# Performance work log

Hardware: AMD Instinct MI355X
Metric: run time of the kernel (lower is better)

The kernel has to match this reference:

```python
import jax, jax.numpy as jnp
import numpy as np

NUM_HEADS = 16
D_K = 64
D_V = 64
D_MODEL = 1024


def setup_inputs() -> dict:
    key = jax.random.key(0)
    ks = jax.random.split(key, 11)
    B, S = 2, 2048
    s = 0.02
    return {
        "Q": jax.random.normal(ks[0], (B, S, D_MODEL), jnp.float32),
        "K": jax.random.normal(ks[1], (B, S, D_MODEL), jnp.float32),
        "V": jax.random.normal(ks[2], (B, S, D_MODEL), jnp.float32),
        "WQ": jax.random.normal(ks[3], (D_MODEL, NUM_HEADS * D_K), jnp.float32) * s,
        "bQ": jnp.zeros((NUM_HEADS * D_K,), jnp.float32),
        "WK": jax.random.normal(ks[4], (D_MODEL, NUM_HEADS * D_K), jnp.float32) * s,
        "bK": jnp.zeros((NUM_HEADS * D_K,), jnp.float32),
        "WV": jax.random.normal(ks[5], (D_MODEL, NUM_HEADS * D_V), jnp.float32) * s,
        "bV": jnp.zeros((NUM_HEADS * D_V,), jnp.float32),
        "WO": jax.random.normal(ks[6], (NUM_HEADS * D_V, D_MODEL), jnp.float32) * s,
        "bO": jnp.zeros((D_MODEL,), jnp.float32),
    }


def reference(Q, K, V, WQ, bQ, WK, bK, WV, bV, WO, bO):
    B = Q.shape[0]
    # linear projections, then split heads: [B, H, S, d]
    q = (Q @ WQ + bQ).reshape(B, -1, NUM_HEADS, D_K).transpose(0, 2, 1, 3)
    k = (K @ WK + bK).reshape(B, -1, NUM_HEADS, D_K).transpose(0, 2, 1, 3)
    v = (V @ WV + bV).reshape(B, -1, NUM_HEADS, D_V).transpose(0, 2, 1, 3)
    # unfused attention: full [B, H, Sq, Sk] score matrix
    scores = jnp.einsum("bhqd,bhkd->bhqk", q, k) / jnp.sqrt(jnp.float32(D_K))
    attn = jax.nn.softmax(scores, axis=-1)  # dropout is identity in eval mode
    out = jnp.einsum("bhqk,bhkd->bhqd", attn, v)
    out = out.transpose(0, 2, 1, 3).reshape(B, -1, NUM_HEADS * D_V)
    return out @ WO + bO
```

## Files before the change

### kernel.cpp

```cpp
#include <hip/hip_runtime.h>
#include <hip/hip_bf16.h>
#include <stdint.h>

#define BATCH 2
#define SEQ   2048
#define NH    16
#define DH    64
#define DM    1024
#define MR    (BATCH * SEQ)

typedef __bf16 bf16_t;
typedef bf16_t bf16x4 __attribute__((ext_vector_type(4)));
typedef bf16_t bf16x8 __attribute__((ext_vector_type(8)));
typedef float  f32x4  __attribute__((ext_vector_type(4)));
typedef float  f32x16 __attribute__((ext_vector_type(16)));

typedef const __attribute__((address_space(1))) void* gas_t;
typedef       __attribute__((address_space(3))) void* las_t;

__device__ __forceinline__ void gload16(const void* g, void* l) {
  __builtin_amdgcn_global_load_lds((gas_t)g, (las_t)l, 16, 0, 0);
}

__device__ __forceinline__ float fast_exp2(float x) {
#if __has_builtin(__builtin_amdgcn_exp2f)
  return __builtin_amdgcn_exp2f(x);
#else
  float r; asm volatile("v_exp_f32 %0, %1\n\ts_nop 1" : "=v"(r) : "v"(x)); return r;
#endif
}

__global__ __launch_bounds__(256) void cvt3_kernel(const float* __restrict__ x0,
                                                   const float* __restrict__ x1,
                                                   const float* __restrict__ x2,
                                                   bf16_t* __restrict__ y0,
                                                   bf16_t* __restrict__ y1,
                                                   bf16_t* __restrict__ y2, int n) {
  const int z = blockIdx.y;
  const float* x = z == 0 ? x0 : (z == 1 ? x1 : x2);
  bf16_t*      y = z == 0 ? y0 : (z == 1 ? y1 : y2);
  int i = (blockIdx.x * 256 + threadIdx.x) * 8;
  if (i + 8 <= n) {
    float4 a = *(const float4*)(x + i);
    float4 b = *(const float4*)(x + i + 4);
    bf16x8 o;
    o[0] = (bf16_t)a.x; o[1] = (bf16_t)a.y; o[2] = (bf16_t)a.z; o[3] = (bf16_t)a.w;
    o[4] = (bf16_t)b.x; o[5] = (bf16_t)b.y; o[6] = (bf16_t)b.z; o[7] = (bf16_t)b.w;
    *(bf16x8*)(y + i) = o;
  }
}

__global__ __launch_bounds__(256) void wtrans4_kernel(const float* __restrict__ W0,
                                                      const float* __restrict__ W1,
                                                      const float* __restrict__ W2,
                                                      const float* __restrict__ W3,
                                                      bf16_t* __restrict__ T0,
                                                      bf16_t* __restrict__ T1,
                                                      bf16_t* __restrict__ T2,
                                                      bf16_t* __restrict__ T3) {
  const int z = blockIdx.z;
  const float* W = z == 0 ? W0 : (z == 1 ? W1 : (z == 2 ? W2 : W3));
  bf16_t*     Wt = z == 0 ? T0 : (z == 1 ? T1 : (z == 2 ? T2 : T3));
  __shared__ bf16_t t[64][65];
  const int c0 = blockIdx.x * 64, r0 = blockIdx.y * 64;
  const int tid = threadIdx.x;
  const int r = tid >> 2, cc = (tid & 3) * 16;
  const float* src = W + (size_t)(r0 + r) * DM + c0 + cc;
#pragma unroll
  for (int i = 0; i < 16; ++i) t[r][cc + i] = (bf16_t)src[i];
  __syncthreads();
  bf16_t* dst = Wt + (size_t)(c0 + r) * DM + r0 + cc;
#pragma unroll
  for (int i = 0; i < 16; ++i) dst[i] = t[cc + i][r];
}

__global__ __launch_bounds__(256) void vtrans_kernel(const bf16_t* __restrict__ v,
                                                     bf16_t* __restrict__ vT) {
  __shared__ bf16_t t[64][65];
  const int s0 = blockIdx.x * 64;
  const int h = blockIdx.y, b = blockIdx.z;
  const int tid = threadIdx.x;
  const int r = tid >> 2, cc = (tid & 3) * 16;
  const bf16_t* src = v + (size_t)(b * SEQ + s0 + r) * DM + h * DH + cc;
#pragma unroll
  for (int i = 0; i < 16; ++i) t[r][cc + i] = src[i];
  __syncthreads();
  bf16_t* dst = vT + (size_t)((b * NH + h) * DH + r) * SEQ + s0 + cc;
#pragma unroll
  for (int i = 0; i < 16; ++i) dst[i] = t[cc + i][r];
}

__global__ __launch_bounds__(256) void gemm3_kernel(
    const bf16_t* __restrict__ A0, const bf16_t* __restrict__ A1,
    const bf16_t* __restrict__ A2,
    const bf16_t* __restrict__ B0, const bf16_t* __restrict__ B1,
    const bf16_t* __restrict__ B2,
    const float* __restrict__ bi0, const float* __restrict__ bi1,
    const float* __restrict__ bi2,
    float s0, float s1, float s2,
    bf16_t* __restrict__ C0, bf16_t* __restrict__ C1, bf16_t* __restrict__ C2) {
  const int z = blockIdx.z;
  const bf16_t* A    = z == 0 ? A0 : (z == 1 ? A1 : A2);
  const bf16_t* Bt   = z == 0 ? B0 : (z == 1 ? B1 : B2);
  const float*  bias = z == 0 ? bi0 : (z == 1 ? bi1 : bi2);
  const float   scale = z == 0 ? s0 : (z == 1 ? s1 : s2);
  bf16_t*       C    = z == 0 ? C0 : (z == 1 ? C1 : C2);
  const int K = DM, N = DM;

  __shared__ __attribute__((aligned(16))) bf16_t As[128 * 64];
  __shared__ __attribute__((aligned(16))) bf16_t Bs[128 * 64];
  const int m0 = blockIdx.x * 128, n0 = blockIdx.y * 128;
  const int tid = threadIdx.x;
  const int wave = tid >> 6, lane = tid & 63;
  const int lm = lane & 15, lg = lane >> 4;
  const int wr = wave >> 1, wc = wave & 1;
  f32x4 acc[4][4];
#pragma unroll
  for (int a = 0; a < 4; ++a)
#pragma unroll
    for (int bb = 0; bb < 4; ++bb) acc[a][bb] = (f32x4){0.f, 0.f, 0.f, 0.f};

  for (int k0 = 0; k0 < K; k0 += 64) {
    __syncthreads();
#pragma unroll
    for (int i = 0; i < 4; ++i) {
      const int c = tid + i * 256;
      const int row = c >> 3, j = c & 7, js = j ^ (row & 7);
      gload16(A  + (size_t)(m0 + row) * K + k0 + js * 8,
              As + (size_t)(wave * 64 + i * 256) * 8);
      gload16(Bt + (size_t)(n0 + row) * K + k0 + js * 8,
              Bs + (size_t)(wave * 64 + i * 256) * 8);
    }
    asm volatile("s_waitcnt vmcnt(0)" ::: "memory");
    __syncthreads();
#pragma unroll
    for (int kk = 0; kk < 2; ++kk) {
      bf16x8 af[4], bfr[4];
#pragma unroll
      for (int t = 0; t < 4; ++t) {
        const int ra = wr * 64 + t * 16 + lm;
        af[t] = *(const bf16x8*)((const char*)As + ra * 128 +
                                 ((kk * 64 + lg * 16) ^ ((ra & 7) << 4)));
        const int rb = wc * 64 + t * 16 + lm;
        bfr[t] = *(const bf16x8*)((const char*)Bs + rb * 128 +
                                  ((kk * 64 + lg * 16) ^ ((rb & 7) << 4)));
      }
      __builtin_amdgcn_s_setprio(1);
#pragma unroll
      for (int mf = 0; mf < 4; ++mf)
#pragma unroll
        for (int nf = 0; nf < 4; ++nf)
          acc[mf][nf] = __builtin_amdgcn_mfma_f32_16x16x32_bf16(af[mf], bfr[nf],
                                                                acc[mf][nf], 0, 0, 0);
      __builtin_amdgcn_s_setprio(0);
    }
  }
#pragma unroll
  for (int mf = 0; mf < 4; ++mf)
#pragma unroll
    for (int nf = 0; nf < 4; ++nf) {
      const int col = n0 + wc * 64 + nf * 16 + lm;
      const float bv = bias[col];
#pragma unroll
      for (int i = 0; i < 4; ++i) {
        const int row = m0 + wr * 64 + mf * 16 + lg * 4 + i;
        C[(size_t)row * N + col] = (bf16_t)((acc[mf][nf][i] + bv) * scale);
      }
    }
}

template <int OUT_BF16>
__global__ __launch_bounds__(256) void gemm_kernel(const bf16_t* __restrict__ A,
                                                   const bf16_t* __restrict__ Bt,
                                                   const float* __restrict__ bias,
                                                   float scale,
                                                   void* __restrict__ Cv,
                                                   int K, int N) {
  __shared__ __attribute__((aligned(16))) bf16_t As[64 * 64];
  __shared__ __attribute__((aligned(16))) bf16_t Bs[128 * 64];
  const int m0 = blockIdx.x * 64, n0 = blockIdx.y * 128;
  const int tid = threadIdx.x;
  const int wave = tid >> 6, lane = tid & 63;
  const int lm = lane & 15, lg = lane >> 4;
  const int wr = wave >> 1, wc = wave & 1;
  f32x4 acc[2][4];
#pragma unroll
  for (int a = 0; a < 2; ++a)
#pragma unroll
    for (int bb = 0; bb < 4; ++bb) acc[a][bb] = (f32x4){0.f, 0.f, 0.f, 0.f};

  for (int k0 = 0; k0 < K; k0 += 64) {
    __syncthreads();
#pragma unroll
    for (int i = 0; i < 2; ++i) {
      const int c = tid + i * 256;
      const int row = c >> 3, j = c & 7, js = j ^ (row & 7);
      gload16(A + (size_t)(m0 + row) * K + k0 + js * 8,
              As + (size_t)(wave * 64 + i * 256) * 8);
    }
#pragma unroll
    for (int i = 0; i < 4; ++i) {
      const int c = tid + i * 256;
      const int row = c >> 3, j = c & 7, js = j ^ (row & 7);
      gload16(Bt + (size_t)(n0 + row) * K + k0 + js * 8,
              Bs + (size_t)(wave * 64 + i * 256) * 8);
    }
    asm volatile("s_waitcnt vmcnt(0)" ::: "memory");
    __syncthreads();
#pragma unroll
    for (int kk = 0; kk < 2; ++kk) {
      bf16x8 af[2], bfr[4];
#pragma unroll
      for (int t = 0; t < 2; ++t) {
        const int ra = wr * 32 + t * 16 + lm;
        af[t] = *(const bf16x8*)((const char*)As + ra * 128 +
                                 ((kk * 64 + lg * 16) ^ ((ra & 7) << 4)));
      }
#pragma unroll
      for (int t = 0; t < 4; ++t) {
        const int rb = wc * 64 + t * 16 + lm;
        bfr[t] = *(const bf16x8*)((const char*)Bs + rb * 128 +
                                  ((kk * 64 + lg * 16) ^ ((rb & 7) << 4)));
      }
      __builtin_amdgcn_s_setprio(1);
#pragma unroll
      for (int mf = 0; mf < 2; ++mf)
#pragma unroll
        for (int nf = 0; nf < 4; ++nf)
          acc[mf][nf] = __builtin_amdgcn_mfma_f32_16x16x32_bf16(af[mf], bfr[nf],
                                                                acc[mf][nf], 0, 0, 0);
      __builtin_amdgcn_s_setprio(0);
    }
  }
#pragma unroll
  for (int mf = 0; mf < 2; ++mf)
#pragma unroll
    for (int nf = 0; nf < 4; ++nf) {
      const int col = n0 + wc * 64 + nf * 16 + lm;
      const float bv = bias[col];
#pragma unroll
      for (int i = 0; i < 4; ++i) {
        const int row = m0 + wr * 32 + mf * 16 + lg * 4 + i;
        const float val = (acc[mf][nf][i] + bv) * scale;
        if (OUT_BF16) ((bf16_t*)Cv)[(size_t)row * N + col] = (bf16_t)val;
        else          ((float*)Cv)[(size_t)row * N + col] = val;
      }
    }
}

__global__ __launch_bounds__(256, 3) void flash_kernel(const bf16_t* __restrict__ q,
                                                       const bf16_t* __restrict__ k,
                                                       const bf16_t* __restrict__ vT,
                                                       bf16_t* __restrict__ o) {
  __shared__ __attribute__((aligned(16))) bf16_t Ks[2][64 * 64];
  __shared__ __attribute__((aligned(16))) bf16_t Vs[2][64 * 64];
  __shared__ __attribute__((aligned(16))) bf16_t Ps[4][32 * 64];
  const int wg = blockIdx.x;
  const int swz = (wg & 7) * 64 + (wg >> 3);
  const int qt = swz & 15, h = (swz >> 4) & 15, b = swz >> 8;
  const int tid = threadIdx.x;
  const int wave = tid >> 6, lane = tid & 63;
  const int lq = lane & 31, hi = lane >> 5;
  char* PsW = (char*)(&Ps[wave][0]);

  const bf16_t* qb = q + (size_t)(b * SEQ + qt * 128 + wave * 32) * DM + h * DH;
  const int c0r = tid >> 3,  c0j = (tid & 7) ^ (c0r & 7);
  const int c1r = c0r + 32,  c1j = (tid & 7) ^ (c1r & 7);
  const bf16_t* kbase = k + (size_t)b * SEQ * DM + h * DH;
  const bf16_t* vbase = vT + (size_t)(b * NH + h) * DH * SEQ;
  const bf16_t* ks0 = kbase + (size_t)c0r * DM + c0j * 8;
  const bf16_t* ks1 = kbase + (size_t)c1r * DM + c1j * 8;
  const bf16_t* vs0 = vbase + (size_t)c0r * SEQ + c0j * 8;
  const bf16_t* vs1 = vbase + (size_t)c1r * SEQ + c1j * 8;

  bf16x8 qf[4];
#pragma unroll
  for (int ds = 0; ds < 4; ++ds)
    qf[ds] = *(const bf16x8*)(qb + (size_t)lq * DM + ds * 16 + hi * 8);

  f32x16 acc[2];
#pragma unroll
  for (int r = 0; r < 16; ++r) { acc[0][r] = 0.f; acc[1][r] = 0.f; }
  float mrun = -1e30f, lrun = 0.f;

  gload16(ks0, &Ks[0][(wave * 64) * 8]);
  gload16(ks1, &Ks[0][(wave * 64 + 256) * 8]);
  gload16(vs0, &Vs[0][(wave * 64) * 8]);
  gload16(vs1, &Vs[0][(wave * 64 + 256) * 8]);

  const int NT = SEQ / 64;
  for (int t = 0; t < NT; ++t) {
    const int cur = t & 1;
    asm volatile("" ::: "memory");
    __builtin_amdgcn_s_barrier();
    if (t + 1 < NT) {
      const int nb = cur ^ 1;
      gload16(ks0 + (size_t)(t + 1) * 64 * DM, &Ks[nb][(wave * 64) * 8]);
      gload16(ks1 + (size_t)(t + 1) * 64 * DM, &Ks[nb][(wave * 64 + 256) * 8]);
      gload16(vs0 + (t + 1) * 64,              &Vs[nb][(wave * 64) * 8]);
      gload16(vs1 + (t + 1) * 64,              &Vs[nb][(wave * 64 + 256) * 8]);
      asm volatile("s_waitcnt vmcnt(4)" ::: "memory");
    } else {
      asm volatile("s_waitcnt vmcnt(0)" ::: "memory");
    }
    __builtin_amdgcn_s_barrier();
    asm volatile("" ::: "memory");

    const char* Kb_ = (const char*)&Ks[cur][0];
    const char* Vb_ = (const char*)&Vs[cur][0];

    f32x16 sc[2];
#pragma unroll
    for (int r = 0; r < 16; ++r) { sc[0][r] = 0.f; sc[1][r] = 0.f; }
    __builtin_amdgcn_s_setprio(1);
#pragma unroll
    for (int ds = 0; ds < 4; ++ds) {
#pragma unroll
      for (int kt = 0; kt < 2; ++kt) {
        const int row = kt * 32 + lq;
        bf16x8 kfrag = *(const bf16x8*)(Kb_ + row * 128 +
                                        ((ds * 32 + hi * 16) ^ ((row & 7) << 4)));
        sc[kt] = __builtin_amdgcn_mfma_f32_32x32x16_bf16(kfrag, qf[ds], sc[kt], 0, 0, 0);
      }
    }
    __builtin_amdgcn_s_setprio(0);

    float ml = sc[0][0];
#pragma unroll
    for (int r = 1; r < 16; ++r) ml = fmaxf(ml, sc[0][r]);
#pragma unroll
    for (int r = 0; r < 16; ++r) ml = fmaxf(ml, sc[1][r]);
    ml = fmaxf(ml, __shfl_xor(ml, 32));
    const bool defer = __all(ml - mrun <= 8.0f);
    const float mn = defer ? mrun : fmaxf(mrun, ml);
#pragma unroll
    for (int kt = 0; kt < 2; ++kt)
#pragma unroll
      for (int r = 0; r < 16; ++r) sc[kt][r] = fast_exp2(sc[kt][r] - mn);
    float s = 0.f;
#pragma unroll
    for (int r = 0; r < 16; ++r) s += sc[0][r] + sc[1][r];
    s += __shfl_xor(s, 32);
    if (defer) {
      lrun += s;
    } else {
      const float alpha = fast_exp2(mrun - mn);
      mrun = mn;
      lrun = lrun * alpha + s;
#pragma unroll
      for (int r = 0; r < 16; ++r) {
        const float ar = __shfl(alpha, (r & 3) + 8 * (r >> 2) + 4 * hi);
        acc[0][r] *= ar;
        acc[1][r] *= ar;
      }
    }

#pragma unroll
    for (int kt = 0; kt < 2; ++kt)
#pragma unroll
      for (int g = 0; g < 4; ++g) {
        bf16x4 pw;
        pw[0] = (bf16_t)sc[kt][4 * g + 0]; pw[1] = (bf16_t)sc[kt][4 * g + 1];
        pw[2] = (bf16_t)sc[kt][4 * g + 2]; pw[3] = (bf16_t)sc[kt][4 * g + 3];
        *(bf16x4*)(PsW + lq * 128 +
                   ((kt * 64 + g * 16 + hi * 8) ^ ((lq & 7) << 4))) = pw;
      }

#pragma unroll
    for (int ks = 0; ks < 4; ++ks) {
      bf16x8 pf = *(const bf16x8*)(PsW + lq * 128 +
                                   ((ks * 32 + hi * 16) ^ ((lq & 7) << 4)));
      __builtin_amdgcn_s_setprio(1);
#pragma unroll
      for (int dt = 0; dt < 2; ++dt) {
        const int row = dt * 32 + lq;
        bf16x8 vfrag = *(const bf16x8*)(Vb_ + row * 128 +
                                        ((ks * 32 + hi * 16) ^ ((row & 7) << 4)));
        acc[dt] = __builtin_amdgcn_mfma_f32_32x32x16_bf16(pf, vfrag, acc[dt], 0, 0, 0);
      }
      __builtin_amdgcn_s_setprio(0);
    }
  }

  const float inv = __builtin_amdgcn_rcpf(lrun);
#pragma unroll
  for (int r = 0; r < 16; ++r) {
    const int qrow = (r & 3) + 8 * (r >> 2) + 4 * hi;
    const float iv = __shfl(inv, qrow);
    const int row = b * SEQ + qt * 128 + wave * 32 + qrow;
#pragma unroll
    for (int dt = 0; dt < 2; ++dt) {
      const int col = h * DH + dt * 32 + lq;
      o[(size_t)row * DM + col] = (bf16_t)(acc[dt][r] * iv);
    }
  }
}

extern "C" void kernel_launch(void* const* d_in, const int* in_sizes, int n_in,
                              void* d_out, int out_size, void* d_ws, size_t ws_size,
                              hipStream_t stream) {
  (void)in_sizes; (void)n_in; (void)out_size; (void)ws_size;
  const float* Q  = (const float*)d_in[0];
  const float* Kx = (const float*)d_in[1];
  const float* V  = (const float*)d_in[2];
  const float* WQ = (const float*)d_in[3];
  const float* bQ = (const float*)d_in[4];
  const float* WK = (const float*)d_in[5];
  const float* bK = (const float*)d_in[6];
  const float* WV = (const float*)d_in[7];
  const float* bV = (const float*)d_in[8];
  const float* WO = (const float*)d_in[9];
  const float* bO = (const float*)d_in[10];

  const size_t MS  = (size_t)MR * DM;
  const size_t WSZ = (size_t)DM * DM;
  bf16_t* ws  = (bf16_t*)d_ws;
  bf16_t* Qb  = ws;
  bf16_t* Kb  = Qb + MS;
  bf16_t* Vb  = Kb + MS;
  bf16_t* WQt = Vb + MS;
  bf16_t* WKt = WQt + WSZ;
  bf16_t* WVt = WKt + WSZ;
  bf16_t* WOt = WVt + WSZ;
  bf16_t* qp  = WOt + WSZ;
  bf16_t* kp  = qp + MS;
  bf16_t* vp  = kp + MS;
  bf16_t* vTb = Qb;
  bf16_t* ao  = Kb;

  const float scale_q = 0.125f * 1.44269504088896340736f;

  cvt3_kernel<<<dim3((unsigned)(MS / 2048), 3), 256, 0, stream>>>(Q, Kx, V, Qb, Kb, Vb, (int)MS);
  wtrans4_kernel<<<dim3(16, 16, 4), 256, 0, stream>>>(WQ, WK, WV, WO, WQt, WKt, WVt, WOt);

  gemm3_kernel<<<dim3(32, 8, 3), 256, 0, stream>>>(Qb, Kb, Vb,
                                                   WQt, WKt, WVt,
                                                   bQ, bK, bV,
                                                   scale_q, 1.0f, 1.0f,
                                                   qp, kp, vp);

  vtrans_kernel<<<dim3(SEQ / 64, NH, BATCH), 256, 0, stream>>>(vp, vTb);
  flash_kernel<<<dim3(512), 256, 0, stream>>>(qp, kp, vTb, ao);
  gemm_kernel<0><<<dim3(MR / 64, DM / 128), 256, 0, stream>>>(ao, WOt, bO, 1.0f, d_out, DM, DM);
}
```

Baseline: 138.6 us.

## Write K/V in MFMA-fragment layout from projection GEMM; load directly to registers in flash

The QKV projection epilogue now writes K and V in a per-head layout that already matches the MFMA fragment order, which makes the separate V-transpose kernel unnecessary. The flash kernel drops its shared-memory K/V double buffering and barriers. Each wave instead loads K and V fragments straight from global memory into registers, with K software-prefetched one tile ahead. The cost is that every wave of a block reloads the same K/V from global or L2 instead of sharing it through LDS, register pressure rises (launch bounds go from 3 to 2 blocks), and the epilogue stores become scattered.

```diff
diff --git a/kernel.cpp b/kernel.cpp
--- a/kernel.cpp
+++ b/kernel.cpp
@@ -74,22 +74,6 @@
   for (int i = 0; i < 16; ++i) dst[i] = t[cc + i][r];
 }
 
-__global__ __launch_bounds__(256) void vtrans_kernel(const bf16_t* __restrict__ v,
-                                                     bf16_t* __restrict__ vT) {
-  __shared__ bf16_t t[64][65];
-  const int s0 = blockIdx.x * 64;
-  const int h = blockIdx.y, b = blockIdx.z;
-  const int tid = threadIdx.x;
-  const int r = tid >> 2, cc = (tid & 3) * 16;
-  const bf16_t* src = v + (size_t)(b * SEQ + s0 + r) * DM + h * DH + cc;
-#pragma unroll
-  for (int i = 0; i < 16; ++i) t[r][cc + i] = src[i];
-  __syncthreads();
-  bf16_t* dst = vT + (size_t)((b * NH + h) * DH + r) * SEQ + s0 + cc;
-#pragma unroll
-  for (int i = 0; i < 16; ++i) dst[i] = t[cc + i][r];
-}
-
 __global__ __launch_bounds__(256) void gemm3_kernel(
     const bf16_t* __restrict__ A0, const bf16_t* __restrict__ A1,
     const bf16_t* __restrict__ A2,
@@ -164,7 +148,23 @@
 #pragma unroll
       for (int i = 0; i < 4; ++i) {
         const int row = m0 + wr * 64 + mf * 16 + lg * 4 + i;
-        C[(size_t)row * N + col] = (bf16_t)((acc[mf][nf][i] + bv) * scale);
+        const float val = (acc[mf][nf][i] + bv) * scale;
+        size_t off;
+        if (z == 0) {
+          off = (size_t)row * N + col;
+        } else {
+          const int bb = row >> 11, s = row & (SEQ - 1);
+          const int hh = col >> 6, d = col & 63;
+          const size_t base = (size_t)(bb * NH + hh) * (SEQ * DH);
+          if (z == 1) {
+            off = base + ((((size_t)(s >> 6) * 2 + ((s >> 5) & 1)) * 4 + (d >> 4)) * 64
+                          + ((d >> 3) & 1) * 32 + (s & 31)) * 8 + (d & 7);
+          } else {
+            off = base + ((((size_t)(s >> 6) * 2 + (d >> 5)) * 4 + ((s >> 4) & 3)) * 64
+                          + ((s >> 3) & 1) * 32 + (d & 31)) * 8 + (s & 7);
+          }
+        }
+        C[off] = (bf16_t)val;
       }
     }
 }
@@ -248,12 +248,84 @@
     }
 }
 
-__global__ __launch_bounds__(256, 3) void flash_kernel(const bf16_t* __restrict__ q,
-                                                       const bf16_t* __restrict__ k,
-                                                       const bf16_t* __restrict__ vT,
+__device__ __forceinline__ void attn_iter5(const bf16x8 (&kf)[8],
+                                           const bf16x8 (&qf)[4],
+                                           const bf16_t* __restrict__ vbt,
+                                           f32x16 (&acc0)[2],
+                                           float& mrun, float& lrun,
+                                           char* __restrict__ PsW,
+                                           int lq, int hi, int lane) {
+  bf16x8 vf[8];
+#pragma unroll
+  for (int i = 0; i < 8; ++i) vf[i] = *(const bf16x8*)(vbt + i * 512);
+
+  f32x16 sc[2];
+#pragma unroll
+  for (int r = 0; r < 16; ++r) { sc[0][r] = 0.f; sc[1][r] = 0.f; }
+  __builtin_amdgcn_s_setprio(1);
+#pragma unroll
+  for (int ds = 0; ds < 4; ++ds) {
+    sc[0] = __builtin_amdgcn_mfma_f32_32x32x16_bf16(kf[ds],     qf[ds], sc[0], 0, 0, 0);
+    sc[1] = __builtin_amdgcn_mfma_f32_32x32x16_bf16(kf[4 + ds], qf[ds], sc[1], 0, 0, 0);
+  }
+  __builtin_amdgcn_s_setprio(0);
+
+  float ml = sc[0][0];
+#pragma unroll
+  for (int r = 1; r < 16; ++r) ml = fmaxf(ml, sc[0][r]);
+#pragma unroll
+  for (int r = 0; r < 16; ++r) ml = fmaxf(ml, sc[1][r]);
+  ml = fmaxf(ml, __shfl_xor(ml, 32));
+  const bool defer = __all(ml - mrun <= 8.0f);
+  const float mn = defer ? mrun : fmaxf(mrun, ml);
+#pragma unroll
+  for (int kt = 0; kt < 2; ++kt)
+#pragma unroll
+    for (int r = 0; r < 16; ++r) sc[kt][r] = fast_exp2(sc[kt][r] - mn);
+  float s = 0.f;
+#pragma unroll
+  for (int r = 0; r < 16; ++r) s += sc[0][r] + sc[1][r];
+  s += __shfl_xor(s, 32);
+  if (defer) {
+    lrun += s;
+  } else {
+    const float alpha = fast_exp2(mrun - mn);
+    mrun = mn;
+    lrun = lrun * alpha + s;
+#pragma unroll
+    for (int r = 0; r < 16; ++r) {
+      const float ar = __shfl(alpha, (r & 3) + 8 * (r >> 2) + 4 * hi);
+      acc0[0][r] *= ar;
+      acc0[1][r] *= ar;
+    }
+  }
+
+#pragma unroll
+  for (int kt = 0; kt < 2; ++kt)
+#pragma unroll
+    for (int g = 0; g < 4; ++g) {
+      bf16x4 pw;
+      pw[0] = (bf16_t)sc[kt][4 * g + 0]; pw[1] = (bf16_t)sc[kt][4 * g + 1];
+      pw[2] = (bf16_t)sc[kt][4 * g + 2]; pw[3] = (bf16_t)sc[kt][4 * g + 3];
+      *(bf16x4*)(PsW + lq * 128 +
+                 ((kt * 64 + g * 16 + hi * 8) ^ ((lq & 7) << 4))) = pw;
+    }
+
+#pragma unroll
+  for (int ks = 0; ks < 4; ++ks) {
+    bf16x8 pf = *(const bf16x8*)(PsW + lq * 128 +
+                                 ((ks * 32 + hi * 16) ^ ((lq & 7) << 4)));
+    __builtin_amdgcn_s_setprio(1);
+    acc0[0] = __builtin_amdgcn_mfma_f32_32x32x16_bf16(pf, vf[ks],     acc0[0], 0, 0, 0);
+    acc0[1] = __builtin_amdgcn_mfma_f32_32x32x16_bf16(pf, vf[4 + ks], acc0[1], 0, 0, 0);
+    __builtin_amdgcn_s_setprio(0);
+  }
+}
+
+__global__ __launch_bounds__(256, 2) void flash_kernel(const bf16_t* __restrict__ q,
+                                                       const bf16_t* __restrict__ kF,
+                                                       const bf16_t* __restrict__ vF,
                                                        bf16_t* __restrict__ o) {
-  __shared__ __attribute__((aligned(16))) bf16_t Ks[2][64 * 64];
-  __shared__ __attribute__((aligned(16))) bf16_t Vs[2][64 * 64];
   __shared__ __attribute__((aligned(16))) bf16_t Ps[4][32 * 64];
   const int wg = blockIdx.x;
   const int swz = (wg & 7) * 64 + (wg >> 3);
@@ -264,14 +336,8 @@
   char* PsW = (char*)(&Ps[wave][0]);
 
   const bf16_t* qb = q + (size_t)(b * SEQ + qt * 128 + wave * 32) * DM + h * DH;
-  const int c0r = tid >> 3,  c0j = (tid & 7) ^ (c0r & 7);
-  const int c1r = c0r + 32,  c1j = (tid & 7) ^ (c1r & 7);
-  const bf16_t* kbase = k + (size_t)b * SEQ * DM + h * DH;
-  const bf16_t* vbase = vT + (size_t)(b * NH + h) * DH * SEQ;
-  const bf16_t* ks0 = kbase + (size_t)c0r * DM + c0j * 8;
-  const bf16_t* ks1 = kbase + (size_t)c1r * DM + c1j * 8;
-  const bf16_t* vs0 = vbase + (size_t)c0r * SEQ + c0j * 8;
-  const bf16_t* vs1 = vbase + (size_t)c1r * SEQ + c1j * 8;
+  const bf16_t* kb = kF + (size_t)(b * NH + h) * (SEQ * DH) + lane * 8;
+  const bf16_t* vb = vF + (size_t)(b * NH + h) * (SEQ * DH) + lane * 8;
 
   bf16x8 qf[4];
 #pragma unroll
@@ -283,103 +349,23 @@
   for (int r = 0; r < 16; ++r) { acc[0][r] = 0.f; acc[1][r] = 0.f; }
   float mrun = -1e30f, lrun = 0.f;
 
-  gload16(ks0, &Ks[0][(wave * 64) * 8]);
-  gload16(ks1, &Ks[0][(wave * 64 + 256) * 8]);
-  gload16(vs0, &Vs[0][(wave * 64) * 8]);
-  gload16(vs1, &Vs[0][(wave * 64 + 256) * 8]);
+  bf16x8 kfA[8], kfB[8];
+#pragma unroll
+  for (int i = 0; i < 8; ++i) kfA[i] = *(const bf16x8*)(kb + i * 512);
 
   const int NT = SEQ / 64;
-  for (int t = 0; t < NT; ++t) {
-    const int cur = t & 1;
-    asm volatile("" ::: "memory");
-    __builtin_amdgcn_s_barrier();
-    if (t + 1 < NT) {
-      const int nb = cur ^ 1;
-      gload16(ks0 + (size_t)(t + 1) * 64 * DM, &Ks[nb][(wave * 64) * 8]);
-      gload16(ks1 + (size_t)(t + 1) * 64 * DM, &Ks[nb][(wave * 64 + 256) * 8]);
-      gload16(vs0 + (t + 1) * 64,              &Vs[nb][(wave * 64) * 8]);
-      gload16(vs1 + (t + 1) * 64,              &Vs[nb][(wave * 64 + 256) * 8]);
-      asm volatile("s_waitcnt vmcnt(4)" ::: "memory");
-    } else {
-      asm volatile("s_waitcnt vmcnt(0)" ::: "memory");
-    }
-    __builtin_amdgcn_s_barrier();
-    asm volatile("" ::: "memory");
-
-    const char* Kb_ = (const char*)&Ks[cur][0];
-    const char* Vb_ = (const char*)&Vs[cur][0];
-
-    f32x16 sc[2];
-#pragma unroll
-    for (int r = 0; r < 16; ++r) { sc[0][r] = 0.f; sc[1][r] = 0.f; }
-    __builtin_amdgcn_s_setprio(1);
-#pragma unroll
-    for (int ds = 0; ds < 4; ++ds) {
-#pragma unroll
-      for (int kt = 0; kt < 2; ++kt) {
-        const int row = kt * 32 + lq;
-        bf16x8 kfrag = *(const bf16x8*)(Kb_ + row * 128 +
-                                        ((ds * 32 + hi * 16) ^ ((row & 7) << 4)));
-        sc[kt] = __builtin_amdgcn_mfma_f32_32x32x16_bf16(kfrag, qf[ds], sc[kt], 0, 0, 0);
-      }
-    }
-    __builtin_amdgcn_s_setprio(0);
-
-    float ml = sc[0][0];
-#pragma unroll
-    for (int r = 1; r < 16; ++r) ml = fmaxf(ml, sc[0][r]);
-#pragma unroll
-    for (int r = 0; r < 16; ++r) ml = fmaxf(ml, sc[1][r]);
-    ml = fmaxf(ml, __shfl_xor(ml, 32));
-    const bool defer = __all(ml - mrun <= 8.0f);
-    const float mn = defer ? mrun : fmaxf(mrun, ml);
-#pragma unroll
-    for (int kt = 0; kt < 2; ++kt)
-#pragma unroll
-      for (int r = 0; r < 16; ++r) sc[kt][r] = fast_exp2(sc[kt][r] - mn);
-    float s = 0.f;
-#pragma unroll
-    for (int r = 0; r < 16; ++r) s += sc[0][r] + sc[1][r];
-    s += __shfl_xor(s, 32);
-    if (defer) {
-      lrun += s;
-    } else {
-      const float alpha = fast_exp2(mrun - mn);
-      mrun = mn;
-      lrun = lrun * alpha + s;
-#pragma unroll
-      for (int r = 0; r < 16; ++r) {
-        const float ar = __shfl(alpha, (r & 3) + 8 * (r >> 2) + 4 * hi);
-        acc[0][r] *= ar;
-        acc[1][r] *= ar;
-      }
-    }
-
-#pragma unroll
-    for (int kt = 0; kt < 2; ++kt)
-#pragma unroll
-      for (int g = 0; g < 4; ++g) {
-        bf16x4 pw;
-        pw[0] = (bf16_t)sc[kt][4 * g + 0]; pw[1] = (bf16_t)sc[kt][4 * g + 1];
-        pw[2] = (bf16_t)sc[kt][4 * g + 2]; pw[3] = (bf16_t)sc[kt][4 * g + 3];
-        *(bf16x4*)(PsW + lq * 128 +
-                   ((kt * 64 + g * 16 + hi * 8) ^ ((lq & 7) << 4))) = pw;
-      }
-
-#pragma unroll
-    for (int ks = 0; ks < 4; ++ks) {
-      bf16x8 pf = *(const bf16x8*)(PsW + lq * 128 +
-                                   ((ks * 32 + hi * 16) ^ ((lq & 7) << 4)));
-      __builtin_amdgcn_s_setprio(1);
-#pragma unroll
-      for (int dt = 0; dt < 2; ++dt) {
-        const int row = dt * 32 + lq;
-        bf16x8 vfrag = *(const bf16x8*)(Vb_ + row * 128 +
-                                        ((ks * 32 + hi * 16) ^ ((row & 7) << 4)));
-        acc[dt] = __builtin_amdgcn_mfma_f32_32x32x16_bf16(pf, vfrag, acc[dt], 0, 0, 0);
-      }
-      __builtin_amdgcn_s_setprio(0);
-    }
+  for (int t = 0; t < NT; t += 2) {
+#pragma unroll
+    for (int i = 0; i < 8; ++i)
+      kfB[i] = *(const bf16x8*)(kb + (size_t)(t + 1) * 4096 + i * 512);
+    attn_iter5(kfA, qf, vb + (size_t)t * 4096, acc, mrun, lrun, PsW, lq, hi, lane);
+    {
+      const int tn = (t + 2 < NT) ? t + 2 : NT - 1;
+#pragma unroll
+      for (int i = 0; i < 8; ++i)
+        kfA[i] = *(const bf16x8*)(kb + (size_t)tn * 4096 + i * 512);
+    }
+    attn_iter5(kfB, qf, vb + (size_t)(t + 1) * 4096, acc, mrun, lrun, PsW, lq, hi, lane);
   }
 
   const float inv = __builtin_amdgcn_rcpf(lrun);
@@ -425,7 +411,6 @@
   bf16_t* qp  = WOt + WSZ;
   bf16_t* kp  = qp + MS;
   bf16_t* vp  = kp + MS;
-  bf16_t* vTb = Qb;
   bf16_t* ao  = Kb;
 
   const float scale_q = 0.125f * 1.44269504088896340736f;
@@ -439,7 +424,6 @@
                                                    scale_q, 1.0f, 1.0f,
                                                    qp, kp, vp);
 
-  vtrans_kernel<<<dim3(SEQ / 64, NH, BATCH), 256, 0, stream>>>(vp, vTb);
-  flash_kernel<<<dim3(512), 256, 0, stream>>>(qp, kp, vTb, ao);
+  flash_kernel<<<dim3(512), 256, 0, stream>>>(qp, kp, vp, ao);
   gemm_kernel<0><<<dim3(MR / 64, DM / 128), 256, 0, stream>>>(ao, WOt, bO, 1.0f, d_out, DM, DM);
 }
```

New measurement: 132.7 us. 1.04x faster.
